# Kernel optimization log

Hardware: AMD Instinct MI355X
Metric: run time of the kernel (lower is better)

The kernel has to match this reference:

```python
import math
import jax, jax.numpy as jnp
import numpy as np

SIGMA_S = 2.0
SIGMA_R = 0.1
KERNEL_SIZE = 9
PAD = KERNEL_SIZE // 2
_COORDS = list(range(-PAD, PAD + 1))
OFFSETS = [(i, j) for i in _COORDS for j in _COORDS]
SPATIAL_W = [math.exp(-((i * i + j * j) / (2.0 * SIGMA_S ** 2))) for i, j in OFFSETS]

B, C, H, W = 16, 1, 768, 1024


def setup_inputs() -> dict:
    key = jax.random.key(0)
    k1, k2, k3 = jax.random.split(key, 3)
    depth = jax.random.uniform(k1, (B, C, H, W), dtype=jnp.float32)
    vals = jax.random.uniform(k2, (B, C, H, W), dtype=jnp.float32)
    mask = jax.random.uniform(k3, (B, C, H, W)) < 0.05
    sparse = jnp.where(mask, vals, jnp.float32(1.0))
    return {"sparse": sparse, "depth": depth}


def reference(sparse, depth):
    pad = PAD
    # sparse padded with the 'missing' sentinel 1.0; depth reflect-padded
    sp = jnp.pad(sparse, ((0, 0), (0, 0), (pad, pad), (pad, pad)), mode="constant", constant_values=1.0)
    dp = jnp.pad(depth, ((0, 0), (0, 0), (pad, pad), (pad, pad)), mode="reflect")
    num = jnp.zeros_like(sparse)
    den = jnp.zeros_like(sparse)
    inv_two_sr2 = 1.0 / (2.0 * SIGMA_R ** 2)
    Hh, Ww = sparse.shape[-2], sparse.shape[-1]
    for (dy, dx), w in zip(OFFSETS, SPATIAL_W):
        sp_shift = sp[..., pad + dy : pad + dy + Hh, pad + dx : pad + dx + Ww]
        dp_shift = dp[..., pad + dy : pad + dy + Hh, pad + dx : pad + dx + Ww]
        valid = (sp_shift != 1.0).astype(sparse.dtype)
        diff = dp_shift - depth
        range_w = jnp.exp(-(diff * diff) * inv_two_sr2)
        w_total = w * range_w * valid
        num = num + w_total * sp_shift
        den = den + w_total
    out = num / (den + 1e-8)
    out = jnp.where(den < 1e-8, jnp.ones_like(out), out)
    return out
```

## Files before the change

### kernel.cpp

```cpp
#include <hip/hip_runtime.h>


#define HH 768
#define WW 1024
#define BB 16
#define CS (-0.18033688011112042f)
#define CR (-72.13475204444817f)

#define TS 68
#define TROWS 31
#define TSIZE (TROWS * TS)
#define TF4   (TSIZE / 4)

typedef float f2 __attribute__((ext_vector_type(2)));

__device__ __forceinline__ int rfl(int x) { return __builtin_amdgcn_readfirstlane(x); }
__device__ __forceinline__ float rlanef(float v, int b) {
    return __int_as_float(__builtin_amdgcn_readlane(__float_as_int(v), b));
}
__device__ __forceinline__ f2 splat(float x) { f2 r; r.x = x; r.y = x; return r; }

__global__ __launch_bounds__(256) void jbf_kernel(
    const float* __restrict__ sparse,
    const float* __restrict__ depth,
    float* __restrict__ out)
{
    __shared__ __align__(16) float Tab[TSIZE];
    const int tid  = (int)threadIdx.x;
    const int lane = tid & 63;
    const int wv   = tid >> 6;

    {
        float4 s; s.x = -1e30f; s.y = -1e30f; s.z = -1e30f; s.w = -1e30f;
        float4* t4 = (float4*)Tab;
        #pragma unroll
        for (int i = 0; i < 3; ++i) {
            const int idx = tid + 256 * i;
            if (idx < TF4) t4[idx] = s;
        }
    }
    __syncthreads();
    if (tid < 81) {
        const int rr = (tid * 57) >> 9;
        const int cc = tid - 9 * rr;
        const float dy = (float)(rr - 4), dx = (float)(cc - 4);
        Tab[(rr + 11) * TS + cc + 19] = CS * fmaf(dy, dy, dx * dx);
    }
    __syncthreads();

    const int tx = rfl(((int)blockIdx.x << 5) + ((wv & 1) << 4));
    const int ty = rfl(((int)blockIdx.y << 4) + ((wv >> 1) << 3));
    const int px0 = rfl(min(max(tx - 4, 0), WW - 24));
    const int py0 = rfl(min(max(ty - 4, 0), HH - 16));
    const int txoff = tx - px0;
    const int tyoff = ty - py0;

    const size_t plane = (size_t)blockIdx.z * (size_t)(HH * WW);
    const float* sp = sparse + plane;
    const float* dp = depth  + plane;

    const int r  = lane >> 2;
    const int c0 = (lane & 3) << 1;
    const float* wbs = sp + (py0 + r) * WW + px0 + c0;
    const float* wbd = dp + (py0 + r) * WW + px0 + c0;
    const f2 s20 = *(const f2*)(wbs);
    const f2 s21 = *(const f2*)(wbs + 8);
    const f2 s22 = *(const f2*)(wbs + 16);
    const f2 d20 = *(const f2*)(wbd);
    const f2 d21 = *(const f2*)(wbd + 8);
    const f2 d22 = *(const f2*)(wbd + 16);

    const int my = lane >> 3, mx = lane & 7;
    const int gy = ty + my, gx = tx + mx;
    const float myd0 = dp[gy * WW + gx];
    const float myd1 = dp[gy * WW + gx + 8];
    f2 nmyd; nmyd.x = -myd0; nmyd.y = -myd1;
    const int clane_w = my * TS + mx;

    f2 numA = splat(0.0f), denA = splat(0.0f);
    f2 numB = splat(0.0f), denB = splat(0.0f);
    const f2 crp = splat(CR);

    const int sbase0 = TS * (15 - tyoff) + (23 - txoff) - 8;

    #pragma unroll
    for (int j = 0; j < 3; ++j) {
        const f2 s2 = (j == 0) ? s20 : (j == 1) ? s21 : s22;
        const f2 d2 = (j == 0) ? d20 : (j == 1) ? d21 : d22;
        #pragma unroll
        for (int k = 0; k < 2; ++k) {
            const float svk = k ? s2.y : s2.x;
            const float dvk = k ? d2.y : d2.x;
            const int sbase = sbase0 + 8 * j + k;
            unsigned long long m = __ballot(svk != 1.0f);
            while (m) {
                const int b0 = (int)__builtin_ctzll(m);
                m &= (m - 1ull);
                {
                    const float sv_e = rlanef(svk, b0);
                    const float dv_e = rlanef(dvk, b0);
                    const int SW = sbase + (b0 >> 2) * TS + ((b0 & 3) << 1);
                    const float* tb = Tab + (SW - clane_w);
                    f2 tp; tp.x = tb[8]; tp.y = tb[0];
                    const f2 diff = nmyd + splat(dv_e);
                    const f2 q = diff * crp;
                    const f2 arg = q * diff + tp;
                    f2 w; w.x = __builtin_amdgcn_exp2f(arg.x);
                    w.y = __builtin_amdgcn_exp2f(arg.y);
                    denA += w;
                    numA += w * splat(sv_e);
                }
                if (m) {
                    const int b1 = (int)__builtin_ctzll(m);
                    m &= (m - 1ull);
                    const float sv_e = rlanef(svk, b1);
                    const float dv_e = rlanef(dvk, b1);
                    const int SW = sbase + (b1 >> 2) * TS + ((b1 & 3) << 1);
                    const float* tb = Tab + (SW - clane_w);
                    f2 tp; tp.x = tb[8]; tp.y = tb[0];
                    const f2 diff = nmyd + splat(dv_e);
                    const f2 q = diff * crp;
                    const f2 arg = q * diff + tp;
                    f2 w; w.x = __builtin_amdgcn_exp2f(arg.x);
                    w.y = __builtin_amdgcn_exp2f(arg.y);
                    denB += w;
                    numB += w * splat(sv_e);
                }
            }
        }
    }

    const float n0 = numA.x + numB.x, n1 = numA.y + numB.y;
    const float e0 = denA.x + denB.x, e1 = denA.y + denB.y;
    float r0 = n0 * __builtin_amdgcn_rcpf(e0 + 1e-8f);
    r0 = (e0 < 1e-8f) ? 1.0f : r0;
    float r1 = n1 * __builtin_amdgcn_rcpf(e1 + 1e-8f);
    r1 = (e1 < 1e-8f) ? 1.0f : r1;
    float* op = out + plane + (size_t)gy * WW + gx;
    op[0] = r0;
    op[8] = r1;
}

extern "C" void kernel_launch(void* const* d_in, const int* in_sizes, int n_in,
                              void* d_out, int out_size, void* d_ws, size_t ws_size,
                              hipStream_t stream)
{
    const float* sparse = (const float*)d_in[0];
    const float* depth  = (const float*)d_in[1];
    float* out = (float*)d_out;
    dim3 grid(WW / 32, HH / 16, BB);
    jbf_kernel<<<grid, dim3(256, 1, 1), 0, stream>>>(sparse, depth, out);
}
```

Before: 174.5 us.

## Process four horizontal tiles per block with double-buffered register prefetch

Each block now covers 128 columns instead of 32, so the grid shrinks by four. Every wave loops over four 16x8 tiles and loads the next tile's sparse and depth values into registers while it computes the current one. This spreads the cost of building the shared spatial-weight table and the block launch over more work, and hides global load latency. In exchange there is less parallelism (fewer blocks) and more register pressure from the second set of buffered values.

```diff
diff --git a/kernel.cpp b/kernel.cpp
--- a/kernel.cpp
+++ b/kernel.cpp
@@ -48,12 +48,10 @@
     }
     __syncthreads();
 
-    const int tx = rfl(((int)blockIdx.x << 5) + ((wv & 1) << 4));
-    const int ty = rfl(((int)blockIdx.y << 4) + ((wv >> 1) << 3));
-    const int px0 = rfl(min(max(tx - 4, 0), WW - 24));
+    const int ty  = rfl(((int)blockIdx.y << 4) + ((wv >> 1) << 3));
     const int py0 = rfl(min(max(ty - 4, 0), HH - 16));
-    const int txoff = tx - px0;
     const int tyoff = ty - py0;
+    const int sbrow = TS * (15 - tyoff);
 
     const size_t plane = (size_t)blockIdx.z * (size_t)(HH * WW);
     const float* sp = sparse + plane;
@@ -61,84 +59,113 @@
 
     const int r  = lane >> 2;
     const int c0 = (lane & 3) << 1;
-    const float* wbs = sp + (py0 + r) * WW + px0 + c0;
-    const float* wbd = dp + (py0 + r) * WW + px0 + c0;
-    const f2 s20 = *(const f2*)(wbs);
-    const f2 s21 = *(const f2*)(wbs + 8);
-    const f2 s22 = *(const f2*)(wbs + 16);
-    const f2 d20 = *(const f2*)(wbd);
-    const f2 d21 = *(const f2*)(wbd + 8);
-    const f2 d22 = *(const f2*)(wbd + 16);
-
     const int my = lane >> 3, mx = lane & 7;
-    const int gy = ty + my, gx = tx + mx;
-    const float myd0 = dp[gy * WW + gx];
-    const float myd1 = dp[gy * WW + gx + 8];
-    f2 nmyd; nmyd.x = -myd0; nmyd.y = -myd1;
+    const int gy = ty + my;
     const int clane_w = my * TS + mx;
-
-    f2 numA = splat(0.0f), denA = splat(0.0f);
-    f2 numB = splat(0.0f), denB = splat(0.0f);
     const f2 crp = splat(CR);
 
-    const int sbase0 = TS * (15 - tyoff) + (23 - txoff) - 8;
+    const int txb = rfl((int)blockIdx.x * 128 + ((wv & 1) << 4));
 
-    #pragma unroll
-    for (int j = 0; j < 3; ++j) {
-        const f2 s2 = (j == 0) ? s20 : (j == 1) ? s21 : s22;
-        const f2 d2 = (j == 0) ? d20 : (j == 1) ? d21 : d22;
-        #pragma unroll
-        for (int k = 0; k < 2; ++k) {
-            const float svk = k ? s2.y : s2.x;
-            const float dvk = k ? d2.y : d2.x;
-            const int sbase = sbase0 + 8 * j + k;
-            unsigned long long m = __ballot(svk != 1.0f);
-            while (m) {
-                const int b0 = (int)__builtin_ctzll(m);
-                m &= (m - 1ull);
-                {
-                    const float sv_e = rlanef(svk, b0);
-                    const float dv_e = rlanef(dvk, b0);
-                    const int SW = sbase + (b0 >> 2) * TS + ((b0 & 3) << 1);
-                    const float* tb = Tab + (SW - clane_w);
-                    f2 tp; tp.x = tb[8]; tp.y = tb[0];
-                    const f2 diff = nmyd + splat(dv_e);
-                    const f2 q = diff * crp;
-                    const f2 arg = q * diff + tp;
-                    f2 w; w.x = __builtin_amdgcn_exp2f(arg.x);
-                    w.y = __builtin_amdgcn_exp2f(arg.y);
-                    denA += w;
-                    numA += w * splat(sv_e);
-                }
-                if (m) {
-                    const int b1 = (int)__builtin_ctzll(m);
-                    m &= (m - 1ull);
-                    const float sv_e = rlanef(svk, b1);
-                    const float dv_e = rlanef(dvk, b1);
-                    const int SW = sbase + (b1 >> 2) * TS + ((b1 & 3) << 1);
-                    const float* tb = Tab + (SW - clane_w);
-                    f2 tp; tp.x = tb[8]; tp.y = tb[0];
-                    const f2 diff = nmyd + splat(dv_e);
-                    const f2 q = diff * crp;
-                    const f2 arg = q * diff + tp;
-                    f2 w; w.x = __builtin_amdgcn_exp2f(arg.x);
-                    w.y = __builtin_amdgcn_exp2f(arg.y);
-                    denB += w;
-                    numB += w * splat(sv_e);
-                }
-            }
-        }
+#define STAGE(TX, PX0, S0, S1, S2, D0, D1, D2, M0, M1)                    \
+    const int PX0 = rfl(min(max((TX) - 4, 0), WW - 24));                  \
+    {                                                                      \
+        const float* wbs = sp + (size_t)(py0 + r) * WW + PX0 + c0;        \
+        const float* wbd = dp + (size_t)(py0 + r) * WW + PX0 + c0;        \
+        S0 = *(const f2*)(wbs);                                            \
+        S1 = *(const f2*)(wbs + 8);                                        \
+        S2 = *(const f2*)(wbs + 16);                                       \
+        D0 = *(const f2*)(wbd);                                            \
+        D1 = *(const f2*)(wbd + 8);                                        \
+        D2 = *(const f2*)(wbd + 16);                                       \
+        M0 = dp[(size_t)gy * WW + (TX) + mx];                              \
+        M1 = dp[(size_t)gy * WW + (TX) + mx + 8];                          \
     }
 
-    const float n0 = numA.x + numB.x, n1 = numA.y + numB.y;
-    const float e0 = denA.x + denB.x, e1 = denA.y + denB.y;
-    float r0 = n0 * __builtin_amdgcn_rcpf(e0 + 1e-8f);
-    r0 = (e0 < 1e-8f) ? 1.0f : r0;
-    float r1 = n1 * __builtin_amdgcn_rcpf(e1 + 1e-8f);
-    r1 = (e1 < 1e-8f) ? 1.0f : r1;
-    float* op = out + plane + (size_t)gy * WW + gx;
-    op[0] = r0;
-    op[8] = r1;
+#define PROCESS(TX, PX0, S0, S1, S2, D0, D1, D2, M0, M1)                  \
+    {                                                                      \
+        const int txoff = (TX) - PX0;                            \
+        const int sbase0 = sbrow + (23 - txoff) - 8;                       \
+        f2 nmyd; nmyd.x = -(M0); nmyd.y = -(M1);                           \
+        f2 numA = splat(0.0f), denA = splat(0.0f);                         \
+        f2 numB = splat(0.0f), denB = splat(0.0f);                         \
+        _Pragma("unroll")                                                  \
+        for (int j = 0; j < 3; ++j) {                                      \
+            const f2 s2 = (j == 0) ? S0 : (j == 1) ? S1 : S2;              \
+            const f2 d2 = (j == 0) ? D0 : (j == 1) ? D1 : D2;              \
+            _Pragma("unroll")                                              \
+            for (int k = 0; k < 2; ++k) {                                  \
+                const float svk = k ? s2.y : s2.x;                         \
+                const float dvk = k ? d2.y : d2.x;                         \
+                const int sbase = sbase0 + 8 * j + k;            \
+                unsigned long long m = __ballot(svk != 1.0f);              \
+                while (m) {                                   \
+                    const int b0 = (int)__builtin_ctzll(m);                \
+                    m &= (m - 1ull);                                       \
+                    {                                                      \
+                        const float sv_e = rlanef(svk, b0);                \
+                        const float dv_e = rlanef(dvk, b0);                \
+                        const int SW = sbase + (b0 >> 2) * TS              \
+                                       + ((b0 & 3) << 1);        \
+                        const float* tb = Tab + (SW - clane_w);            \
+                        f2 tp; tp.x = tb[8]; tp.y = tb[0];   \
+                        const f2 diff = nmyd + splat(dv_e);                \
+                        const f2 q = diff * crp;                           \
+                        const f2 arg = q * diff + tp;          \
+                        f2 w; w.x = __builtin_amdgcn_exp2f(arg.x);         \
+                        w.y = __builtin_amdgcn_exp2f(arg.y);               \
+                        denA += w;                                         \
+                        numA += w * splat(sv_e);               \
+                    }                                                      \
+                    if (m) {                                  \
+                        const int b1 = (int)__builtin_ctzll(m);            \
+                        m &= (m - 1ull);                                   \
+                        const float sv_e = rlanef(svk, b1);                \
+                        const float dv_e = rlanef(dvk, b1);                \
+                        const int SW = sbase + (b1 >> 2) * TS              \
+                                       + ((b1 & 3) << 1);                  \
+                        const float* tb = Tab + (SW - clane_w);            \
+                        f2 tp; tp.x = tb[8]; tp.y = tb[0];                 \
+                        const f2 diff = nmyd + splat(dv_e);                \
+                        const f2 q = diff * crp;                           \
+                        const f2 arg = q * diff + tp;                      \
+                        f2 w; w.x = __builtin_amdgcn_exp2f(arg.x);         \
+                        w.y = __builtin_amdgcn_exp2f(arg.y);               \
+                        denB += w;                                         \
+                        numB += w * splat(sv_e);                           \
+                    }                                                      \
+                }                                                          \
+            }                                                              \
+        }                                                                  \
+        const float n0 = numA.x + numB.x, n1 = numA.y + numB.y;            \
+        const float e0 = denA.x + denB.x, e1 = denA.y + denB.y;            \
+        float r0 = n0 * __builtin_amdgcn_rcpf(e0 + 1e-8f);                 \
+        r0 = (e0 < 1e-8f) ? 1.0f : r0;                                     \
+        float r1 = n1 * __builtin_amdgcn_rcpf(e1 + 1e-8f);                 \
+        r1 = (e1 < 1e-8f) ? 1.0f : r1;                                     \
+        float* op = out + plane + (size_t)gy * WW + (TX) + mx;             \
+        op[0] = r0;                                                        \
+        op[8] = r1;                                                        \
+    }
+
+    f2 sA0, sA1, sA2, dA0, dA1, dA2; float mA0, mA1;
+    f2 sB0, sB1, sB2, dB0, dB1, dB2; float mB0, mB1;
+
+    const int tx0 = txb;
+    const int tx1 = txb + 32;
+    const int tx2 = txb + 64;
+    const int tx3 = txb + 96;
+
+    STAGE(tx0, px0a, sA0, sA1, sA2, dA0, dA1, dA2, mA0, mA1)
+    STAGE(tx1, px0b, sB0, sB1, sB2, dB0, dB1, dB2, mB0, mB1)
+    PROCESS(tx0, px0a, sA0, sA1, sA2, dA0, dA1, dA2, mA0, mA1)
+    STAGE(tx2, px0c, sA0, sA1, sA2, dA0, dA1, dA2, mA0, mA1)
+    PROCESS(tx1, px0b, sB0, sB1, sB2, dB0, dB1, dB2, mB0, mB1)
+    STAGE(tx3, px0d, sB0, sB1, sB2, dB0, dB1, dB2, mB0, mB1)
+    PROCESS(tx2, px0c, sA0, sA1, sA2, dA0, dA1, dA2, mA0, mA1)
+    PROCESS(tx3, px0d, sB0, sB1, sB2, dB0, dB1, dB2, mB0, mB1)
+
+#undef STAGE
+#undef PROCESS
 }
 
 extern "C" void kernel_launch(void* const* d_in, const int* in_sizes, int n_in,
@@ -148,6 +175,6 @@
     const float* sparse = (const float*)d_in[0];
     const float* depth  = (const float*)d_in[1];
     float* out = (float*)d_out;
-    dim3 grid(WW / 32, HH / 16, BB);
+    dim3 grid(WW / 128, HH / 16, BB);
     jbf_kernel<<<grid, dim3(256, 1, 1), 0, stream>>>(sparse, depth, out);
 }
```

Result: no change. 175.5 us (+0.5%).

## Process four 8x8 tiles per wave with double-buffered loads and scalar accumulation

Applied to the files above, without the earlier changes.

Each wave now covers four 8x8 output tiles, one output per lane per tile, instead of one 8x16 tile with two outputs per lane. The 16x16 neighbourhood for the next tile is loaded as float4 while the current one is processed, a two-stage software pipeline. The grid is halved, the shared spatial-weight table shrinks, and the table setup cost is spread over more work. The price is more ballot/readlane loop overhead per output, because each sparse neighbour now feeds a single pixel rather than two, and neighbourhood loads overlap more between tiles.

```diff
diff --git a/kernel.cpp b/kernel.cpp
--- a/kernel.cpp
+++ b/kernel.cpp
@@ -7,18 +7,15 @@
 #define CS (-0.18033688011112042f)
 #define CR (-72.13475204444817f)
 
-#define TS 68
+#define TS 40
 #define TROWS 31
 #define TSIZE (TROWS * TS)
 #define TF4   (TSIZE / 4)
-
-typedef float f2 __attribute__((ext_vector_type(2)));
 
 __device__ __forceinline__ int rfl(int x) { return __builtin_amdgcn_readfirstlane(x); }
 __device__ __forceinline__ float rlanef(float v, int b) {
     return __int_as_float(__builtin_amdgcn_readlane(__float_as_int(v), b));
 }
-__device__ __forceinline__ f2 splat(float x) { f2 r; r.x = x; r.y = x; return r; }
 
 __global__ __launch_bounds__(256) void jbf_kernel(
     const float* __restrict__ sparse,
@@ -34,7 +31,7 @@
         float4 s; s.x = -1e30f; s.y = -1e30f; s.z = -1e30f; s.w = -1e30f;
         float4* t4 = (float4*)Tab;
         #pragma unroll
-        for (int i = 0; i < 3; ++i) {
+        for (int i = 0; i < 2; ++i) {
             const int idx = tid + 256 * i;
             if (idx < TF4) t4[idx] = s;
         }
@@ -44,101 +41,108 @@
         const int rr = (tid * 57) >> 9;
         const int cc = tid - 9 * rr;
         const float dy = (float)(rr - 4), dx = (float)(cc - 4);
-        Tab[(rr + 11) * TS + cc + 19] = CS * fmaf(dy, dy, dx * dx);
+        Tab[(rr + 11) * TS + cc + 11] = CS * fmaf(dy, dy, dx * dx);
     }
     __syncthreads();
 
-    const int tx = rfl(((int)blockIdx.x << 5) + ((wv & 1) << 4));
-    const int ty = rfl(((int)blockIdx.y << 4) + ((wv >> 1) << 3));
-    const int px0 = rfl(min(max(tx - 4, 0), WW - 24));
+    const int wr = wv >> 1, wc = wv & 1;
+    const int my = lane >> 3, mx = lane & 7;
+    const int sr = lane >> 2, sc = (lane & 3) << 2;
+
+    const int ty  = rfl(((int)blockIdx.y << 4) + (wr << 3));
     const int py0 = rfl(min(max(ty - 4, 0), HH - 16));
-    const int txoff = tx - px0;
     const int tyoff = ty - py0;
+    const int gy = ty + my;
 
     const size_t plane = (size_t)blockIdx.z * (size_t)(HH * WW);
     const float* sp = sparse + plane;
     const float* dp = depth  + plane;
 
-    const int r  = lane >> 2;
-    const int c0 = (lane & 3) << 1;
-    const float* wbs = sp + (py0 + r) * WW + px0 + c0;
-    const float* wbd = dp + (py0 + r) * WW + px0 + c0;
-    const f2 s20 = *(const f2*)(wbs);
-    const f2 s21 = *(const f2*)(wbs + 8);
-    const f2 s22 = *(const f2*)(wbs + 16);
-    const f2 d20 = *(const f2*)(wbd);
-    const f2 d21 = *(const f2*)(wbd + 8);
-    const f2 d22 = *(const f2*)(wbd + 16);
+    const int clane = my * TS + mx;
+    const float crf = CR;
 
-    const int my = lane >> 3, mx = lane & 7;
-    const int gy = ty + my, gx = tx + mx;
-    const float myd0 = dp[gy * WW + gx];
-    const float myd1 = dp[gy * WW + gx + 8];
-    f2 nmyd; nmyd.x = -myd0; nmyd.y = -myd1;
-    const int clane_w = my * TS + mx;
+    const int txb = rfl((int)blockIdx.x * 64 + (wc << 3));
 
-    f2 numA = splat(0.0f), denA = splat(0.0f);
-    f2 numB = splat(0.0f), denB = splat(0.0f);
-    const f2 crp = splat(CR);
-
-    const int sbase0 = TS * (15 - tyoff) + (23 - txoff) - 8;
-
-    #pragma unroll
-    for (int j = 0; j < 3; ++j) {
-        const f2 s2 = (j == 0) ? s20 : (j == 1) ? s21 : s22;
-        const f2 d2 = (j == 0) ? d20 : (j == 1) ? d21 : d22;
-        #pragma unroll
-        for (int k = 0; k < 2; ++k) {
-            const float svk = k ? s2.y : s2.x;
-            const float dvk = k ? d2.y : d2.x;
-            const int sbase = sbase0 + 8 * j + k;
-            unsigned long long m = __ballot(svk != 1.0f);
-            while (m) {
-                const int b0 = (int)__builtin_ctzll(m);
-                m &= (m - 1ull);
-                {
-                    const float sv_e = rlanef(svk, b0);
-                    const float dv_e = rlanef(dvk, b0);
-                    const int SW = sbase + (b0 >> 2) * TS + ((b0 & 3) << 1);
-                    const float* tb = Tab + (SW - clane_w);
-                    f2 tp; tp.x = tb[8]; tp.y = tb[0];
-                    const f2 diff = nmyd + splat(dv_e);
-                    const f2 q = diff * crp;
-                    const f2 arg = q * diff + tp;
-                    f2 w; w.x = __builtin_amdgcn_exp2f(arg.x);
-                    w.y = __builtin_amdgcn_exp2f(arg.y);
-                    denA += w;
-                    numA += w * splat(sv_e);
-                }
-                if (m) {
-                    const int b1 = (int)__builtin_ctzll(m);
-                    m &= (m - 1ull);
-                    const float sv_e = rlanef(svk, b1);
-                    const float dv_e = rlanef(dvk, b1);
-                    const int SW = sbase + (b1 >> 2) * TS + ((b1 & 3) << 1);
-                    const float* tb = Tab + (SW - clane_w);
-                    f2 tp; tp.x = tb[8]; tp.y = tb[0];
-                    const f2 diff = nmyd + splat(dv_e);
-                    const f2 q = diff * crp;
-                    const f2 arg = q * diff + tp;
-                    f2 w; w.x = __builtin_amdgcn_exp2f(arg.x);
-                    w.y = __builtin_amdgcn_exp2f(arg.y);
-                    denB += w;
-                    numB += w * splat(sv_e);
-                }
-            }
-        }
+#define STAGE(TX, PX0, S4, D4, MD)                                        \
+    const int PX0 = rfl(min(max((TX) - 4, 0), WW - 16));                  \
+    {                                                                      \
+        const size_t wb = (size_t)(py0 + sr) * WW + PX0 + sc;             \
+        S4 = *(const float4*)(sp + wb);                                    \
+        D4 = *(const float4*)(dp + wb);                                    \
+        MD = dp[(size_t)gy * WW + (TX) + mx];                              \
     }
 
-    const float n0 = numA.x + numB.x, n1 = numA.y + numB.y;
-    const float e0 = denA.x + denB.x, e1 = denA.y + denB.y;
-    float r0 = n0 * __builtin_amdgcn_rcpf(e0 + 1e-8f);
-    r0 = (e0 < 1e-8f) ? 1.0f : r0;
-    float r1 = n1 * __builtin_amdgcn_rcpf(e1 + 1e-8f);
-    r1 = (e1 < 1e-8f) ? 1.0f : r1;
-    float* op = out + plane + (size_t)gy * WW + gx;
-    op[0] = r0;
-    op[8] = r1;
+#define PROCESS(TX, PX0, S4, D4, MD)                                      \
+    {                                                                      \
+        const int txoff = (TX) - PX0;                            \
+        const int sbase0 = TS * (15 - tyoff) + (15 - txoff);               \
+        const float md = (MD);                                             \
+        float numA = 0.f, denA = 0.f, numB = 0.f, denB = 0.f;              \
+        _Pragma("unroll")                                                  \
+        for (int k = 0; k < 4; ++k) {                                      \
+            const float svk = (k == 0) ? S4.x : (k == 1) ? S4.y            \
+                            : (k == 2) ? S4.z : S4.w;                      \
+            const float dvk = (k == 0) ? D4.x : (k == 1) ? D4.y            \
+                            : (k == 2) ? D4.z : D4.w;                      \
+            const int sbk = sbase0 + k;                          \
+            unsigned long long m = __ballot(svk != 1.0f);                  \
+            while (m) {                                       \
+                const int b0 = (int)__builtin_ctzll(m);                    \
+                m &= (m - 1ull);                                           \
+                {                                                          \
+                    const float sv0 = rlanef(svk, b0);                     \
+                    const float dv0 = rlanef(dvk, b0);                     \
+                    const int SW = sbk + (b0 >> 2) * TS                    \
+                                   + ((b0 & 3) << 2);            \
+                    const float tp = Tab[SW - clane];     \
+                    const float diff = dv0 - md;                           \
+                    const float arg = fmaf(diff * crf, diff, tp);          \
+                    const float w = __builtin_amdgcn_exp2f(arg);           \
+                    denA += w;                                             \
+                    numA = fmaf(sv0, w, numA);                             \
+                }                                                          \
+                if (m) {                                      \
+                    const int b1 = (int)__builtin_ctzll(m);                \
+                    m &= (m - 1ull);                                       \
+                    const float sv1 = rlanef(svk, b1);                     \
+                    const float dv1 = rlanef(dvk, b1);                     \
+                    const int SW = sbk + (b1 >> 2) * TS                    \
+                                   + ((b1 & 3) << 2);                      \
+                    const float tp = Tab[SW - clane];                      \
+                    const float diff = dv1 - md;                           \
+                    const float arg = fmaf(diff * crf, diff, tp);          \
+                    const float w = __builtin_amdgcn_exp2f(arg);           \
+                    denB += w;                                             \
+                    numB = fmaf(sv1, w, numB);                             \
+                }                                                          \
+            }                                                              \
+        }                                                                  \
+        const float n = numA + numB;                                       \
+        const float e = denA + denB;                                       \
+        float rr2 = n * __builtin_amdgcn_rcpf(e + 1e-8f);                  \
+        rr2 = (e < 1e-8f) ? 1.0f : rr2;                                    \
+        out[plane + (size_t)gy * WW + (TX) + mx] = rr2;                    \
+    }
+
+    float4 s4A, d4A; float mdA;
+    float4 s4B, d4B; float mdB;
+
+    const int tx0 = txb;
+    const int tx1 = txb + 16;
+    const int tx2 = txb + 32;
+    const int tx3 = txb + 48;
+
+    STAGE(tx0, px0a, s4A, d4A, mdA)
+    STAGE(tx1, px0b, s4B, d4B, mdB)
+    PROCESS(tx0, px0a, s4A, d4A, mdA)
+    STAGE(tx2, px0c, s4A, d4A, mdA)
+    PROCESS(tx1, px0b, s4B, d4B, mdB)
+    STAGE(tx3, px0d, s4B, d4B, mdB)
+    PROCESS(tx2, px0c, s4A, d4A, mdA)
+    PROCESS(tx3, px0d, s4B, d4B, mdB)
+
+#undef STAGE
+#undef PROCESS
 }
 
 extern "C" void kernel_launch(void* const* d_in, const int* in_sizes, int n_in,
@@ -148,6 +152,6 @@
     const float* sparse = (const float*)d_in[0];
     const float* depth  = (const float*)d_in[1];
     float* out = (float*)d_out;
-    dim3 grid(WW / 32, HH / 16, BB);
+    dim3 grid(WW / 64, HH / 16, BB);
     jbf_kernel<<<grid, dim3(256, 1, 1), 0, stream>>>(sparse, depth, out);
 }
```

New measurement: 173.3 us. About the same (-0.7%).
